# Performance work log

Measured on AMD Instinct MI355X. Metric: run time of the kernel, lower is better.

## Reference

```python
import jax, jax.numpy as jnp
import numpy as np

B, D, K = 65536, 128, 4096
BETA = 0.25


def setup_inputs() -> dict:
    key = jax.random.key(0)
    k1, k2 = jax.random.split(key)
    encoding = jax.random.normal(k1, (B, D), dtype=jnp.float32)
    # nn.Embedding weight initialized uniform(-1/K, 1/K)
    embedding_weight = jax.random.uniform(
        k2, (K, D), dtype=jnp.float32, minval=-1.0 / K, maxval=1.0 / K
    )
    return {"encoding": encoding, "embedding_weight": embedding_weight}


def reference(encoding, embedding_weight):
    # encode: cdist(p=2).min(dim=-1)[1]  -> argmin of squared euclidean distance
    # dist2[b,k] = ||x_b||^2 - 2 x_b . e_k + ||e_k||^2   (B,K)
    x2 = jnp.sum(encoding * encoding, axis=-1, keepdims=True)          # (B,1)
    e2 = jnp.sum(embedding_weight * embedding_weight, axis=-1)        # (K,)
    xe = jnp.einsum('bd,kd->bk', encoding, embedding_weight)          # (B,K)
    dist2 = x2 - 2.0 * xe + e2[None, :]
    quantized_index = jnp.argmin(dist2, axis=-1)                      # (B,) int

    # one-hot matmul gather == direct gather
    quantized_embedding = embedding_weight[quantized_index]           # (B,D)

    commitment_loss = jnp.mean(
        (encoding - jax.lax.stop_gradient(quantized_embedding)) ** 2
    )
    embedding_loss = jnp.mean(
        (quantized_embedding - jax.lax.stop_gradient(encoding)) ** 2
    )
    vq_loss = commitment_loss * BETA + embedding_loss

    # straight-through estimator
    quantized_st = encoding + jax.lax.stop_gradient(quantized_embedding - encoding)
    return (quantized_index, quantized_st, vq_loss, embedding_loss, commitment_loss)
```

## Files before the change

### kernel.cpp

```cpp
#include <hip/hip_runtime.h>
#include <cfloat>

#define B_N 65536
#define D_N 128
#define K_N 4096
#define NKT (K_N / 64)
#define NOUTB ((B_N * D_N) / 1024)

#define MARGIN_ACC 5e-5f
#define CAP 768

typedef __bf16 bf16x8 __attribute__((ext_vector_type(8)));
typedef float  f32x4  __attribute__((ext_vector_type(4)));

static constexpr size_t WS_E2D   = 0;
static constexpr size_t WS_E2F   = WS_E2D + 8 * (size_t)K_N;
static constexpr size_t WS_PART  = WS_E2F + 4 * (size_t)K_N;
static constexpr size_t WS_EPREP = WS_PART + 8 * (size_t)NOUTB;
static constexpr size_t WS_NEED  = WS_EPREP + (size_t)NKT * 16384;

__device__ __forceinline__ float f32mul(float a, float b) { return (float)((double)a * (double)b); }
__device__ __forceinline__ float f32add(float a, float b) { return (float)((double)a + (double)b); }
__device__ __forceinline__ float f32sub(float a, float b) { return (float)((double)a - (double)b); }

__device__ __forceinline__ unsigned fkey(float f) {
    unsigned u = __float_as_uint(f);
    return (u & 0x80000000u) ? ~u : (u | 0x80000000u);
}
__device__ __forceinline__ float finv(unsigned k) {
    return __uint_as_float((k & 0x80000000u) ? (k ^ 0x80000000u) : ~k);
}

__device__ __forceinline__ void casMin64(unsigned long long* p, unsigned long long v) {
    unsigned long long old = *p;
    while (v < old) {
        unsigned long long prev = atomicCAS(p, old, v);
        if (prev == old) break;
        old = prev;
    }
}

__device__ __forceinline__ float np_score(const float4* __restrict__ xr,
                                          const float4* __restrict__ er,
                                          float x2, float e2) {
    float l0 = 0.f, l1 = 0.f, l2 = 0.f, l3 = 0.f;
#pragma unroll
    for (int f = 0; f < 32; ++f) {
        float4 xv = xr[f];
        float4 ev = er[f];
        l0 = f32add(l0, f32mul(xv.x, ev.x));
        l1 = f32add(l1, f32mul(xv.y, ev.y));
        l2 = f32add(l2, f32mul(xv.z, ev.z));
        l3 = f32add(l3, f32mul(xv.w, ev.w));
    }
    float xe = f32add(f32add(l0, l2), f32add(l1, l3));
    float S  = f32sub(x2, 2.0f * xe);
    return f32add(S, e2);
}

__global__ void k_setup(const float* __restrict__ e, double* __restrict__ e2d,
                        float* __restrict__ e2f, int full) {
    int k = blockIdx.x * blockDim.x + threadIdx.x;
    if (k < K_N) {
        const float* row = e + (size_t)k * D_N;
        double s = 0.0;
        for (int d = 0; d < D_N; ++d) { double v = (double)row[d]; s += v * v; }
        e2d[k] = s;
        if (full) e2f[k] = (float)s;
    }
}

__global__ void k_prep_e(const float* __restrict__ e, unsigned char* __restrict__ eprep) {
    const int g = blockIdx.x * 256 + threadIdx.x;
    const int kt   = g >> 10;
    const int q    = g & 1023;
    const int w    = q >> 8;
    const int c    = (q >> 6) & 3;
    const int lane = q & 63;
    const int r  = kt * 64 + w * 16 + (lane & 15);
    const int d0 = c * 32 + (lane >> 4) * 8;
    const float* src = e + (size_t)r * D_N + d0;
    float4 a = *(const float4*)src;
    float4 b = *(const float4*)(src + 4);
    bf16x8 h;
    h[0] = (__bf16)a.x; h[1] = (__bf16)a.y; h[2] = (__bf16)a.z; h[3] = (__bf16)a.w;
    h[4] = (__bf16)b.x; h[5] = (__bf16)b.y; h[6] = (__bf16)b.z; h[7] = (__bf16)b.w;
    *(bf16x8*)(eprep + (size_t)g * 16) = h;
}

#define MFMA_BF16 __builtin_amdgcn_mfma_f32_16x16x32_bf16

#define TILE_STEP(C0, C1, C2, C3, N0, N1, N2, N3, KT)                               \
    do {                                                                            \
        const int k0 = (KT) * 64 + w * 16;                                          \
        float4 e2v = *(const float4*)(e2f + k0 + lq * 4);                           \
        if ((KT) + 1 < NKT) {                                                       \
            const unsigned char* bp = ebase + (size_t)((KT) + 1) * 16384;           \
            N0 = *(const bf16x8*)(bp);                                              \
            N1 = *(const bf16x8*)(bp + 1024);                                       \
            N2 = *(const bf16x8*)(bp + 2048);                                       \
            N3 = *(const bf16x8*)(bp + 3072);                                       \
        }                                                                           \
        f32x4 ainit = {0.5f * e2v.x, 0.5f * e2v.y, 0.5f * e2v.z, 0.5f * e2v.w};     \
        f32x4 a0 = MFMA_BF16(C0, bxh[0][0], ainit, 0, 0, 0);                        \
        f32x4 a1 = MFMA_BF16(C0, bxh[1][0], ainit, 0, 0, 0);                        \
        a0 = MFMA_BF16(C0, bxl[0][0], a0, 0, 0, 0);                                 \
        a1 = MFMA_BF16(C0, bxl[1][0], a1, 0, 0, 0);                                 \
        a0 = MFMA_BF16(C1, bxh[0][1], a0, 0, 0, 0);                                 \
        a1 = MFMA_BF16(C1, bxh[1][1], a1, 0, 0, 0);                                 \
        a0 = MFMA_BF16(C1, bxl[0][1], a0, 0, 0, 0);                                 \
        a1 = MFMA_BF16(C1, bxl[1][1], a1, 0, 0, 0);                                 \
        a0 = MFMA_BF16(C2, bxh[0][2], a0, 0, 0, 0);                                 \
        a1 = MFMA_BF16(C2, bxh[1][2], a1, 0, 0, 0);                                 \
        a0 = MFMA_BF16(C2, bxl[0][2], a0, 0, 0, 0);                                 \
        a1 = MFMA_BF16(C2, bxl[1][2], a1, 0, 0, 0);                                 \
        a0 = MFMA_BF16(C3, bxh[0][3], a0, 0, 0, 0);                                 \
        a1 = MFMA_BF16(C3, bxh[1][3], a1, 0, 0, 0);                                 \
        a0 = MFMA_BF16(C3, bxl[0][3], a0, 0, 0, 0);                                 \
        a1 = MFMA_BF16(C3, bxl[1][3], a1, 0, 0, 0);                                 \
        float q0 = fminf(fminf(a0[0], a0[1]), fminf(a0[2], a0[3]));                 \
        float q1 = fminf(fminf(a1[0], a1[1]), fminf(a1[2], a1[3]));                 \
        rm0 = fminf(rm0, q0);                                                       \
        rm1 = fminf(rm1, q1);                                                       \
        if ((KT) == 0 || ((KT) & 3) == 3) {                                         \
            float s0 = fminf(rm0, __shfl_xor(rm0, 16));                             \
            s0 = fminf(s0, __shfl_xor(s0, 32));                                     \
            float s1 = fminf(rm1, __shfl_xor(rm1, 16));                             \
            s1 = fminf(s1, __shfl_xor(s1, 32));                                     \
            if (lq == 0) {                                                          \
                unsigned kk0 = fkey(s0);                                            \
                if (kk0 < m1key[lm]) atomicMin(&m1key[lm], kk0);                    \
                unsigned kk1 = fkey(s1);                                            \
                if (kk1 < m1key[16 + lm]) atomicMin(&m1key[16 + lm], kk1);          \
            }                                                                       \
            if ((KT) == 0) __syncthreads();                                         \
            thr0 = finv(m1key[lm]) + MARGIN_ACC;                                    \
            thr1 = finv(m1key[16 + lm]) + MARGIN_ACC;                               \
        }                                                                           \
        if (q0 < thr0) {                                                            \
            _Pragma("unroll")                                                       \
            for (int r = 0; r < 4; ++r)                                             \
                if (a0[r] < thr0) {                                                 \
                    int pos = atomicAdd(&cnt, 1);                                   \
                    if (pos < CAP) {                                                \
                        candT[pos] = a0[r];                                         \
                        candKX[pos] = ((unsigned)(k0 + lq * 4 + r) << 5) | lm;      \
                    } else rowbad[lm] = 1;                                          \
                }                                                                   \
        }                                                                           \
        if (q1 < thr1) {                                                            \
            _Pragma("unroll")                                                       \
            for (int r = 0; r < 4; ++r)                                             \
                if (a1[r] < thr1) {                                                 \
                    int pos = atomicAdd(&cnt, 1);                                   \
                    if (pos < CAP) {                                                \
                        candT[pos] = a1[r];                                         \
                        candKX[pos] = ((unsigned)(k0 + lq * 4 + r) << 5) | (16 + lm); \
                    } else rowbad[16 + lm] = 1;                                     \
                }                                                                   \
        }                                                                           \
    } while (0)

__launch_bounds__(256, 4)
__global__ void k_scores_mfma(const float* __restrict__ x, const float* __restrict__ e,
                              const float* __restrict__ e2f,
                              const unsigned char* __restrict__ eprep, float* __restrict__ out) {
    __shared__ unsigned m1key[32];
    __shared__ float    x2s[32];
    __shared__ unsigned long long finkey[32];
    __shared__ float    candT[CAP];
    __shared__ unsigned candKX[CAP];
    __shared__ int      rowbad[32];
    __shared__ int cnt;

    const int tid = threadIdx.x;
    const int w   = tid >> 6;
    const int l   = tid & 63;
    const int lq  = l >> 4;
    const int lm  = l & 15;
    const int row0 = blockIdx.x * 32;

    if (tid < 32) { m1key[tid] = 0xFFFFFFFFu; finkey[tid] = ~0ULL; rowbad[tid] = 0; }
    if (tid == 0) cnt = 0;

    bf16x8 bxh[2][4], bxl[2][4];
    double sx[2] = {0.0, 0.0};
#pragma unroll
    for (int f = 0; f < 2; ++f)
#pragma unroll
        for (int d = 0; d < 4; ++d) {
            const float* px = x + (size_t)(row0 + f * 16 + lm) * D_N + d * 32 + lq * 8;
            float4 a = *(const float4*)px;
            float4 b = *(const float4*)(px + 4);
            float vv[8] = {a.x, a.y, a.z, a.w, b.x, b.y, b.z, b.w};
            bf16x8 h, lo;
#pragma unroll
            for (int j = 0; j < 8; ++j) {
                float v = -vv[j];
                __bf16 hb = (__bf16)v;
                h[j] = hb;
                lo[j] = (__bf16)(v - (float)hb);
                sx[f] += (double)vv[j] * (double)vv[j];
            }
            bxh[f][d] = h; bxl[f][d] = lo;
        }
#pragma unroll
    for (int f = 0; f < 2; ++f) {
        sx[f] += __shfl_xor(sx[f], 16);
        sx[f] += __shfl_xor(sx[f], 32);
    }
    if (w == 0 && l < 16) { x2s[l] = (float)sx[0]; x2s[16 + l] = (float)sx[1]; }
    __syncthreads();

    const unsigned char* ebase = eprep + (size_t)w * 4096 + (size_t)l * 16;

    bf16x8 c0 = *(const bf16x8*)(ebase);
    bf16x8 c1 = *(const bf16x8*)(ebase + 1024);
    bf16x8 c2 = *(const bf16x8*)(ebase + 2048);
    bf16x8 c3 = *(const bf16x8*)(ebase + 3072);
    bf16x8 n0, n1, n2, n3;

    float rm0 = FLT_MAX, rm1 = FLT_MAX;
    float thr0 = FLT_MAX, thr1 = FLT_MAX;

    for (int kt = 0; kt < NKT; kt += 2) {
        TILE_STEP(c0, c1, c2, c3, n0, n1, n2, n3, kt);
        TILE_STEP(n0, n1, n2, n3, c0, c1, c2, c3, kt + 1);
    }
    __syncthreads();

    const int n = min(cnt, CAP);
    for (int i = tid; i < n; i += 256) {
        float tf = candT[i];
        unsigned kx = candKX[i];
        int xl = kx & 31;
        int k = kx >> 5;
        if (tf < finv(m1key[xl]) + MARGIN_ACC) {
            float tn = np_score((const float4*)(x + (size_t)(row0 + xl) * D_N),
                                (const float4*)(e + (size_t)k * D_N),
                                x2s[xl], e2f[k]);
            casMin64(&finkey[xl], ((unsigned long long)fkey(tn) << 32) | (unsigned)k);
        }
    }
    for (int ls = 0; ls < 32; ++ls) {
        if (!rowbad[ls]) continue;
        for (int k = tid; k < K_N; k += 256) {
            float tn = np_score((const float4*)(x + (size_t)(row0 + ls) * D_N),
                                (const float4*)(e + (size_t)k * D_N),
                                x2s[ls], e2f[k]);
            casMin64(&finkey[ls], ((unsigned long long)fkey(tn) << 32) | (unsigned)k);
        }
    }
    __syncthreads();
    if (tid < 32) out[row0 + tid] = (float)(unsigned)(finkey[tid] & 0xFFFFFFFFull);
}

__launch_bounds__(256, 2)
__global__ void k_scores_old(const float* __restrict__ x, const float* __restrict__ e,
                             const double* __restrict__ e2d, float* __restrict__ out) {
    __shared__ float4 Xs[64 * 32];
    __shared__ float4 Es[64 * 32];
    __shared__ float  rowm1[64], rowm2[64];
    __shared__ int    rowidx[64];
    __shared__ double dbuf[256];
    __shared__ float  rv[256];
    __shared__ int    ri[256];

    const int tid = threadIdx.x;
    const int rg = tid >> 4;
    const int cg = tid & 15;
    const int row0 = blockIdx.x * 64;

    const float4* xg = (const float4*)x + (size_t)row0 * 32;
#pragma unroll
    for (int it = 0; it < 8; ++it) {
        int p = tid + it * 256;
        int r = p >> 5, f = p & 31;
        Xs[r * 32 + (f ^ ((r >> 2) & 7))] = xg[p];
    }

    float m1[4], m2[4];
    int   i1[4];
#pragma unroll
    for (int i = 0; i < 4; ++i) { m1[i] = FLT_MAX; m2[i] = FLT_MAX; i1[i] = 0; }

    for (int kt = 0; kt < K_N / 64; ++kt) {
        __syncthreads();
        const float4* eg = (const float4*)e + (size_t)kt * 64 * 32;
#pragma unroll
        for (int it = 0; it < 8; ++it) {
            int p = tid + it * 256;
            int r = p >> 5, f = p & 31;
            Es[r * 32 + (f ^ ((r >> 2) & 7))] = eg[p];
        }
        __syncthreads();

        float acc[4][4];
#pragma unroll
        for (int i = 0; i < 4; ++i)
#pragma unroll
            for (int j = 0; j < 4; ++j) acc[i][j] = 0.f;

#pragma unroll 4
        for (int f = 0; f < 32; ++f) {
            float4 xv[4], ev[4];
#pragma unroll
            for (int i = 0; i < 4; ++i) xv[i] = Xs[(rg * 4 + i) * 32 + (f ^ (rg & 7))];
#pragma unroll
            for (int j = 0; j < 4; ++j) ev[j] = Es[(cg * 4 + j) * 32 + (f ^ (cg & 7))];
#pragma unroll
            for (int i = 0; i < 4; ++i)
#pragma unroll
                for (int j = 0; j < 4; ++j) {
                    acc[i][j] = fmaf(xv[i].x, ev[j].x, acc[i][j]);
                    acc[i][j] = fmaf(xv[i].y, ev[j].y, acc[i][j]);
                    acc[i][j] = fmaf(xv[i].z, ev[j].z, acc[i][j]);
                    acc[i][j] = fmaf(xv[i].w, ev[j].w, acc[i][j]);
                }
        }

#pragma unroll
        for (int j = 0; j < 4; ++j) {
            int k = kt * 64 + cg * 4 + j;
            float e2f = (float)e2d[k];
#pragma unroll
            for (int i = 0; i < 4; ++i) {
                float t = fmaf(-2.f, acc[i][j], e2f);
                if (t < m1[i]) { m2[i] = m1[i]; m1[i] = t; i1[i] = k; }
                else if (t < m2[i]) m2[i] = t;
            }
        }
    }

#pragma unroll
    for (int off = 1; off < 16; off <<= 1) {
#pragma unroll
        for (int i = 0; i < 4; ++i) {
            float om1 = __shfl_xor(m1[i], off);
            float om2 = __shfl_xor(m2[i], off);
            int   oi1 = __shfl_xor(i1[i], off);
            bool take = (om1 < m1[i]) || (om1 == m1[i] && oi1 < i1[i]);
            float nm2 = take ? fminf(m1[i], om2) : fminf(om1, m2[i]);
            if (take) { m1[i] = om1; i1[i] = oi1; }
            m2[i] = nm2;
        }
    }

    if (cg == 0) {
#pragma unroll
        for (int i = 0; i < 4; ++i) {
            int ls = rg * 4 + i;
            rowm1[ls] = m1[i];
            rowm2[ls] = m2[i];
            rowidx[ls] = i1[i];
        }
    }
    __syncthreads();

    for (int ls = 0; ls < 64; ++ls) {
        if (!(rowm2[ls] - rowm1[ls] < 1e-4f)) continue;

        const int row = row0 + ls;
        const int sw = (ls >> 2) & 7;

        double p = 0.0;
        if (tid < D_N) { float v = x[(size_t)row * D_N + tid]; p = (double)v * (double)v; }
        dbuf[tid] = p;
        __syncthreads();
        for (int s = 128; s > 0; s >>= 1) {
            if (tid < s) dbuf[tid] += dbuf[tid + s];
            __syncthreads();
        }
        const float x2f = (float)dbuf[0];
        const double thr = (double)rowm1[ls] + 2e-4;

        float bt = FLT_MAX; int bk = 0;
        for (int k = tid; k < K_N; k += 256) {
            const float4* eg4 = (const float4*)(e + (size_t)k * D_N);
            double dot = 0.0;
#pragma unroll
            for (int f = 0; f < 32; ++f) {
                float4 ev = eg4[f];
                float4 xv = Xs[ls * 32 + (f ^ sw)];
                dot += (double)xv.x * (double)ev.x + (double)xv.y * (double)ev.y
                     + (double)xv.z * (double)ev.z + (double)xv.w * (double)ev.w;
            }
            double t64 = e2d[k] - 2.0 * dot;
            if (t64 < thr) {
                float l0 = 0.f, l1 = 0.f, l2 = 0.f, l3 = 0.f;
#pragma unroll
                for (int f = 0; f < 32; ++f) {
                    float4 ev = eg4[f];
                    float4 xv = Xs[ls * 32 + (f ^ sw)];
                    l0 = f32add(l0, f32mul(xv.x, ev.x));
                    l1 = f32add(l1, f32mul(xv.y, ev.y));
                    l2 = f32add(l2, f32mul(xv.z, ev.z));
                    l3 = f32add(l3, f32mul(xv.w, ev.w));
                }
                float xe = f32add(f32add(l0, l2), f32add(l1, l3));
                float S  = f32sub(x2f, 2.0f * xe);
                float t  = f32add(S, (float)e2d[k]);
                if (t < bt) { bt = t; bk = k; }
            }
        }
        rv[tid] = bt; ri[tid] = bk;
        __syncthreads();
        for (int s = 128; s > 0; s >>= 1) {
            if (tid < s) {
                float ov = rv[tid + s]; int oi = ri[tid + s];
                if (ov < rv[tid] || (ov == rv[tid] && oi < ri[tid])) {
                    rv[tid] = ov; ri[tid] = oi;
                }
            }
            __syncthreads();
        }
        if (tid == 0) rowidx[ls] = ri[0];
        __syncthreads();
    }

    if (tid < 64) out[row0 + tid] = (float)rowidx[tid];
}

__global__ void k_output(const float* __restrict__ x, const float* __restrict__ e,
                         float* __restrict__ out, double* __restrict__ partials) {
    __shared__ double red[256];
    const int tid = threadIdx.x;
    const size_t base = (size_t)blockIdx.x * 1024;
    const size_t elem = base + (size_t)tid * 4;
    const int row = (int)(elem >> 7);
    const int idx = (int)out[row];

    float4 xv = *(const float4*)(x + elem);
    float4 qv = *(const float4*)(e + (size_t)idx * D_N + (elem & 127));
    float4 st;
    st.x = xv.x + (qv.x - xv.x);
    st.y = xv.y + (qv.y - xv.y);
    st.z = xv.z + (qv.z - xv.z);
    st.w = xv.w + (qv.w - xv.w);
    *(float4*)(out + (size_t)B_N + elem) = st;

    double dx = (double)xv.x - (double)qv.x;
    double dy = (double)xv.y - (double)qv.y;
    double dz = (double)xv.z - (double)qv.z;
    double dw = (double)xv.w - (double)qv.w;
    red[tid] = dx * dx + dy * dy + dz * dz + dw * dw;
    __syncthreads();
    for (int s = 128; s > 0; s >>= 1) {
        if (tid < s) red[tid] += red[tid + s];
        __syncthreads();
    }
    if (tid == 0) partials[blockIdx.x] = red[0];
}

__global__ void k_final(const double* __restrict__ partials, float* __restrict__ out) {
    __shared__ double red[256];
    const int tid = threadIdx.x;
    double s = 0.0;
    for (int i = tid; i < NOUTB; i += 256) s += partials[i];
    red[tid] = s;
    __syncthreads();
    for (int st = 128; st > 0; st >>= 1) {
        if (tid < st) red[tid] += red[tid + st];
        __syncthreads();
    }
    if (tid == 0) {
        double mse = red[0] / ((double)B_N * (double)D_N);
        float c = (float)mse;
        float emb = (float)mse;
        float vq = c * 0.25f + emb;
        size_t o = (size_t)B_N + (size_t)B_N * D_N;
        out[o + 0] = vq;
        out[o + 1] = emb;
        out[o + 2] = c;
    }
}

extern "C" void kernel_launch(void* const* d_in, const int* in_sizes, int n_in,
                              void* d_out, int out_size, void* d_ws, size_t ws_size,
                              hipStream_t stream) {
    const float* x = (const float*)d_in[0];
    const float* e = (const float*)d_in[1];
    float* out = (float*)d_out;

    char* ws = (char*)d_ws;
    double* e2d      = (double*)(ws + WS_E2D);
    float*  e2f      = (float*)(ws + WS_E2F);
    double* partials = (double*)(ws + WS_PART);
    unsigned char* eprep = (unsigned char*)(ws + WS_EPREP);

    const bool full = (ws_size >= WS_NEED);

    k_setup<<<K_N / 256, 256, 0, stream>>>(e, e2d, e2f, full ? 1 : 0);
    if (full) {
        k_prep_e<<<(K_N * 16) / 256, 256, 0, stream>>>(e, eprep);
        k_scores_mfma<<<B_N / 32, 256, 0, stream>>>(x, e, e2f, eprep, out);
    } else {
        k_scores_old<<<B_N / 64, 256, 0, stream>>>(x, e, e2d, out);
    }
    k_output<<<NOUTB, 256, 0, stream>>>(x, e, out, partials);
    k_final<<<1, 256, 0, stream>>>(partials, out);
}
```

Measured before the change: 212.1 us.

## Drop bf16 low-part split for x and process 64 rows per block

Stops splitting the encoding into high and low bf16 parts, so each tile needs half as many MFMA ops per row. The coarser approximate score is covered by a wider candidate margin, and exact fp32 rescoring of the candidates still decides the final index. Each block now handles 64 rows instead of 32, so every embedding tile loaded is reused across twice as many rows, and the block count halves. The wider margin and larger block admit more candidates, which risks overflowing the candidate buffer and falling back to full-row rescans.

New measurement: 290.8 us. 1.37x slower.

```diff
diff --git a/kernel.cpp b/kernel.cpp
--- a/kernel.cpp
+++ b/kernel.cpp
@@ -7,7 +7,7 @@
 #define NKT (K_N / 64)
 #define NOUTB ((B_N * D_N) / 1024)
 
-#define MARGIN_ACC 5e-5f
+#define FAST_MARGIN 1e-4f
 #define CAP 768
 
 typedef __bf16 bf16x8 __attribute__((ext_vector_type(8)));
@@ -101,63 +101,54 @@
             N2 = *(const bf16x8*)(bp + 2048);                                       \
             N3 = *(const bf16x8*)(bp + 3072);                                       \
         }                                                                           \
-        f32x4 ainit = {0.5f * e2v.x, 0.5f * e2v.y, 0.5f * e2v.z, 0.5f * e2v.w};     \
-        f32x4 a0 = MFMA_BF16(C0, bxh[0][0], ainit, 0, 0, 0);                        \
-        f32x4 a1 = MFMA_BF16(C0, bxh[1][0], ainit, 0, 0, 0);                        \
-        a0 = MFMA_BF16(C0, bxl[0][0], a0, 0, 0, 0);                                 \
-        a1 = MFMA_BF16(C0, bxl[1][0], a1, 0, 0, 0);                                 \
-        a0 = MFMA_BF16(C1, bxh[0][1], a0, 0, 0, 0);                                 \
-        a1 = MFMA_BF16(C1, bxh[1][1], a1, 0, 0, 0);                                 \
-        a0 = MFMA_BF16(C1, bxl[0][1], a0, 0, 0, 0);                                 \
-        a1 = MFMA_BF16(C1, bxl[1][1], a1, 0, 0, 0);                                 \
-        a0 = MFMA_BF16(C2, bxh[0][2], a0, 0, 0, 0);                                 \
-        a1 = MFMA_BF16(C2, bxh[1][2], a1, 0, 0, 0);                                 \
-        a0 = MFMA_BF16(C2, bxl[0][2], a0, 0, 0, 0);                                 \
-        a1 = MFMA_BF16(C2, bxl[1][2], a1, 0, 0, 0);                                 \
-        a0 = MFMA_BF16(C3, bxh[0][3], a0, 0, 0, 0);                                 \
-        a1 = MFMA_BF16(C3, bxh[1][3], a1, 0, 0, 0);                                 \
-        a0 = MFMA_BF16(C3, bxl[0][3], a0, 0, 0, 0);                                 \
-        a1 = MFMA_BF16(C3, bxl[1][3], a1, 0, 0, 0);                                 \
-        float q0 = fminf(fminf(a0[0], a0[1]), fminf(a0[2], a0[3]));                 \
-        float q1 = fminf(fminf(a1[0], a1[1]), fminf(a1[2], a1[3]));                 \
-        rm0 = fminf(rm0, q0);                                                       \
-        rm1 = fminf(rm1, q1);                                                       \
+        f32x4 acc[4] = {};                                                          \
+        _Pragma("unroll")                                                           \
+        for (int f = 0; f < 4; ++f) acc[f] = MFMA_BF16(C0, bxh[f][0], acc[f], 0, 0, 0); \
+        _Pragma("unroll")                                                           \
+        for (int f = 0; f < 4; ++f) acc[f] = MFMA_BF16(C1, bxh[f][1], acc[f], 0, 0, 0); \
+        _Pragma("unroll")                                                           \
+        for (int f = 0; f < 4; ++f) acc[f] = MFMA_BF16(C2, bxh[f][2], acc[f], 0, 0, 0); \
+        _Pragma("unroll")                                                           \
+        for (int f = 0; f < 4; ++f) acc[f] = MFMA_BF16(C3, bxh[f][3], acc[f], 0, 0, 0); \
+        float tv[4][4];                                                             \
+        float qm[4];                                                                \
+        _Pragma("unroll")                                                           \
+        for (int f = 0; f < 4; ++f) {                                               \
+            tv[f][0] = fmaf(2.0f, acc[f][0], e2v.x);                                \
+            tv[f][1] = fmaf(2.0f, acc[f][1], e2v.y);                                \
+            tv[f][2] = fmaf(2.0f, acc[f][2], e2v.z);                                \
+            tv[f][3] = fmaf(2.0f, acc[f][3], e2v.w);                                \
+            qm[f] = fminf(fminf(tv[f][0], tv[f][1]), fminf(tv[f][2], tv[f][3]));    \
+            rm[f] = fminf(rm[f], qm[f]);                                            \
+        }                                                                           \
         if ((KT) == 0 || ((KT) & 3) == 3) {                                         \
-            float s0 = fminf(rm0, __shfl_xor(rm0, 16));                             \
-            s0 = fminf(s0, __shfl_xor(s0, 32));                                     \
-            float s1 = fminf(rm1, __shfl_xor(rm1, 16));                             \
-            s1 = fminf(s1, __shfl_xor(s1, 32));                                     \
-            if (lq == 0) {                                                          \
-                unsigned kk0 = fkey(s0);                                            \
-                if (kk0 < m1key[lm]) atomicMin(&m1key[lm], kk0);                    \
-                unsigned kk1 = fkey(s1);                                            \
-                if (kk1 < m1key[16 + lm]) atomicMin(&m1key[16 + lm], kk1);          \
+            _Pragma("unroll")                                                       \
+            for (int f = 0; f < 4; ++f) {                                           \
+                float s0 = fminf(rm[f], __shfl_xor(rm[f], 16));                     \
+                s0 = fminf(s0, __shfl_xor(s0, 32));                                 \
+                if (lq == 0) {                                                      \
+                    unsigned kk = fkey(s0);                                         \
+                    if (kk < m1key[f * 16 + lm]) atomicMin(&m1key[f * 16 + lm], kk);\
+                }                                                                   \
             }                                                                       \
             if ((KT) == 0) __syncthreads();                                         \
-            thr0 = finv(m1key[lm]) + MARGIN_ACC;                                    \
-            thr1 = finv(m1key[16 + lm]) + MARGIN_ACC;                               \
+            _Pragma("unroll")                                                       \
+            for (int f = 0; f < 4; ++f) thr[f] = finv(m1key[f * 16 + lm]) + FAST_MARGIN; \
         }                                                                           \
-        if (q0 < thr0) {                                                            \
-            _Pragma("unroll")                                                       \
-            for (int r = 0; r < 4; ++r)                                             \
-                if (a0[r] < thr0) {                                                 \
-                    int pos = atomicAdd(&cnt, 1);                                   \
-                    if (pos < CAP) {                                                \
-                        candT[pos] = a0[r];                                         \
-                        candKX[pos] = ((unsigned)(k0 + lq * 4 + r) << 5) | lm;      \
-                    } else rowbad[lm] = 1;                                          \
-                }                                                                   \
-        }                                                                           \
-        if (q1 < thr1) {                                                            \
-            _Pragma("unroll")                                                       \
-            for (int r = 0; r < 4; ++r)                                             \
-                if (a1[r] < thr1) {                                                 \
-                    int pos = atomicAdd(&cnt, 1);                                   \
-                    if (pos < CAP) {                                                \
-                        candT[pos] = a1[r];                                         \
-                        candKX[pos] = ((unsigned)(k0 + lq * 4 + r) << 5) | (16 + lm); \
-                    } else rowbad[16 + lm] = 1;                                     \
-                }                                                                   \
+        _Pragma("unroll")                                                           \
+        for (int f = 0; f < 4; ++f) {                                               \
+            if (qm[f] < thr[f]) {                                                   \
+                const int xl = f * 16 + lm;                                         \
+                _Pragma("unroll")                                                   \
+                for (int r = 0; r < 4; ++r)                                         \
+                    if (tv[f][r] < thr[f]) {                                        \
+                        int pos = atomicAdd(&cnt, 1);                               \
+                        if (pos < CAP) {                                            \
+                            candT[pos] = tv[f][r];                                  \
+                            candKX[pos] = ((unsigned)(k0 + lq * 4 + r) << 6) | (unsigned)xl; \
+                        } else rowbad[xl] = 1;                                      \
+                    }                                                               \
+            }                                                                       \
         }                                                                           \
     } while (0)
 
@@ -165,12 +156,12 @@
 __global__ void k_scores_mfma(const float* __restrict__ x, const float* __restrict__ e,
                               const float* __restrict__ e2f,
                               const unsigned char* __restrict__ eprep, float* __restrict__ out) {
-    __shared__ unsigned m1key[32];
-    __shared__ float    x2s[32];
-    __shared__ unsigned long long finkey[32];
+    __shared__ unsigned m1key[64];
+    __shared__ float    x2s[64];
+    __shared__ unsigned long long finkey[64];
     __shared__ float    candT[CAP];
     __shared__ unsigned candKX[CAP];
-    __shared__ int      rowbad[32];
+    __shared__ int      rowbad[64];
     __shared__ int cnt;
 
     const int tid = threadIdx.x;
@@ -178,38 +169,38 @@
     const int l   = tid & 63;
     const int lq  = l >> 4;
     const int lm  = l & 15;
-    const int row0 = blockIdx.x * 32;
-
-    if (tid < 32) { m1key[tid] = 0xFFFFFFFFu; finkey[tid] = ~0ULL; rowbad[tid] = 0; }
+    const int row0 = blockIdx.x * 64;
+
+    if (tid < 64) { m1key[tid] = 0xFFFFFFFFu; finkey[tid] = ~0ULL; rowbad[tid] = 0; }
     if (tid == 0) cnt = 0;
 
-    bf16x8 bxh[2][4], bxl[2][4];
-    double sx[2] = {0.0, 0.0};
-#pragma unroll
-    for (int f = 0; f < 2; ++f)
+    bf16x8 bxh[4][4];
+    double sx[4] = {0.0, 0.0, 0.0, 0.0};
+#pragma unroll
+    for (int f = 0; f < 4; ++f)
 #pragma unroll
         for (int d = 0; d < 4; ++d) {
             const float* px = x + (size_t)(row0 + f * 16 + lm) * D_N + d * 32 + lq * 8;
             float4 a = *(const float4*)px;
             float4 b = *(const float4*)(px + 4);
             float vv[8] = {a.x, a.y, a.z, a.w, b.x, b.y, b.z, b.w};
-            bf16x8 h, lo;
+            bf16x8 h;
 #pragma unroll
             for (int j = 0; j < 8; ++j) {
-                float v = -vv[j];
-                __bf16 hb = (__bf16)v;
-                h[j] = hb;
-                lo[j] = (__bf16)(v - (float)hb);
+                h[j] = (__bf16)(-vv[j]);
                 sx[f] += (double)vv[j] * (double)vv[j];
             }
-            bxh[f][d] = h; bxl[f][d] = lo;
-        }
-#pragma unroll
-    for (int f = 0; f < 2; ++f) {
+            bxh[f][d] = h;
+        }
+#pragma unroll
+    for (int f = 0; f < 4; ++f) {
         sx[f] += __shfl_xor(sx[f], 16);
         sx[f] += __shfl_xor(sx[f], 32);
     }
-    if (w == 0 && l < 16) { x2s[l] = (float)sx[0]; x2s[16 + l] = (float)sx[1]; }
+    if (w == 0 && l < 16) {
+#pragma unroll
+        for (int f = 0; f < 4; ++f) x2s[f * 16 + l] = (float)sx[f];
+    }
     __syncthreads();
 
     const unsigned char* ebase = eprep + (size_t)w * 4096 + (size_t)l * 16;
@@ -220,8 +211,8 @@
     bf16x8 c3 = *(const bf16x8*)(ebase + 3072);
     bf16x8 n0, n1, n2, n3;
 
-    float rm0 = FLT_MAX, rm1 = FLT_MAX;
-    float thr0 = FLT_MAX, thr1 = FLT_MAX;
+    float rm[4]  = {FLT_MAX, FLT_MAX, FLT_MAX, FLT_MAX};
+    float thr[4] = {FLT_MAX, FLT_MAX, FLT_MAX, FLT_MAX};
 
     for (int kt = 0; kt < NKT; kt += 2) {
         TILE_STEP(c0, c1, c2, c3, n0, n1, n2, n3, kt);
@@ -233,16 +224,16 @@
     for (int i = tid; i < n; i += 256) {
         float tf = candT[i];
         unsigned kx = candKX[i];
-        int xl = kx & 31;
-        int k = kx >> 5;
-        if (tf < finv(m1key[xl]) + MARGIN_ACC) {
+        int xl = kx & 63;
+        int k = kx >> 6;
+        if (tf < finv(m1key[xl]) + FAST_MARGIN) {
             float tn = np_score((const float4*)(x + (size_t)(row0 + xl) * D_N),
                                 (const float4*)(e + (size_t)k * D_N),
                                 x2s[xl], e2f[k]);
             casMin64(&finkey[xl], ((unsigned long long)fkey(tn) << 32) | (unsigned)k);
         }
     }
-    for (int ls = 0; ls < 32; ++ls) {
+    for (int ls = 0; ls < 64; ++ls) {
         if (!rowbad[ls]) continue;
         for (int k = tid; k < K_N; k += 256) {
             float tn = np_score((const float4*)(x + (size_t)(row0 + ls) * D_N),
@@ -252,7 +243,7 @@
         }
     }
     __syncthreads();
-    if (tid < 32) out[row0 + tid] = (float)(unsigned)(finkey[tid] & 0xFFFFFFFFull);
+    if (tid < 64) out[row0 + tid] = (float)(unsigned)(finkey[tid] & 0xFFFFFFFFull);
 }
 
 __launch_bounds__(256, 2)
@@ -493,7 +484,7 @@
     k_setup<<<K_N / 256, 256, 0, stream>>>(e, e2d, e2f, full ? 1 : 0);
     if (full) {
         k_prep_e<<<(K_N * 16) / 256, 256, 0, stream>>>(e, eprep);
-        k_scores_mfma<<<B_N / 32, 256, 0, stream>>>(x, e, e2f, eprep, out);
+        k_scores_mfma<<<B_N / 64, 256, 0, stream>>>(x, e, e2f, eprep, out);
     } else {
         k_scores_old<<<B_N / 64, 256, 0, stream>>>(x, e, e2d, out);
     }
```
